# Performance work log

Measured on AMD Instinct MI355X. Metric: run time of the kernel, lower is better.

## Reference

```python
import jax, jax.numpy as jnp
import numpy as np

B = 10      # number of interacting objects
NDIM = 2    # self.n: position/velocity dimensionality

# Edge list equivalent to rel_rec/rel_send one-hot matrices (edges grouped by receiver)
_rec_idx, _send_idx = np.where(~np.eye(B, dtype=bool))


def _mlp(x, W0, b0, W1, b1, W2, b2):
    # MLP with 2 hidden softplus layers, linear output
    h = jax.nn.softplus(x @ W0 + b0)
    h = jax.nn.softplus(h @ W1 + b1)
    return h @ W2 + b2


def setup_inputs() -> dict:
    key = jax.random.key(0)
    ks = jax.random.split(key, 7)
    N = 8192            # trajectories per batch
    H = 128             # hidden width of self-dynamics MLP
    Hi = 128            # hidden width of interaction MLP
    nin = 2 * NDIM      # self MLP input dim (pos+vel)
    nout = 2 * NDIM     # n_f_out for order=1
    nin_i = 3 * NDIM    # interaction MLP input dim (p1-p2, v1, v2)
    w = lambda k, shp: jax.random.normal(k, shp, jnp.float32) / np.float32(np.sqrt(shp[0]))
    return {
        "z": jax.random.normal(ks[0], (N * B, 2 * NDIM), jnp.float32),
        "fW0": w(ks[1], (nin, H)),   "fb0": jnp.zeros((H,), jnp.float32),
        "fW1": w(ks[2], (H, H)),     "fb1": jnp.zeros((H,), jnp.float32),
        "fW2": w(ks[3], (H, nout)),  "fb2": jnp.zeros((nout,), jnp.float32),
        "iW0": w(ks[4], (nin_i, Hi)),"ib0": jnp.zeros((Hi,), jnp.float32),
        "iW1": w(ks[5], (Hi, Hi)),   "ib1": jnp.zeros((Hi,), jnp.float32),
        "iW2": w(ks[6], (Hi, nout)), "ib2": jnp.zeros((nout,), jnp.float32),
    }


def reference(z, fW0, fb0, fW1, fb1, fW2, fb2, iW0, ib0, iW1, ib1, iW2, ib2):
    # One evaluation of the ODE vector field (order=1, n_aug_dyn=n_aug_st=0).
    n = NDIM
    NB = z.shape[0]
    N = NB // B
    dz_self = _mlp(z, fW0, fb0, fW1, fb1, fW2, fb2)            # [N*B, 2n]
    z3 = z.reshape(N, B, 2 * n)
    recv = z3[:, _rec_idx]                                     # [N, B(B-1), 2n] gather (node2edge)
    send = z3[:, _send_idx]
    # odefint input: (p_recv - p_send, v_recv, v_send)  -> [N, B(B-1), 3n]
    inp = jnp.concatenate([recv[..., :n] - send[..., :n], recv[..., n:], send[..., n:]], -1)
    dz_int = _mlp(inp, iW0, ib0, iW1, ib1, iW2, ib2)           # [N, B(B-1), 2n]
    dz_int = dz_int.reshape(N, B, B - 1, 2 * n).sum(2)         # sum over senders per receiver
    dz = dz_self.reshape(N, B, 2 * n) + dz_int
    return dz.reshape(NB, 2 * n)
```

## Files before the change

kernel.cpp:

```cpp
#include <hip/hip_runtime.h>
#include <hip/hip_bf16.h>

#define NDIM 2
#define BB 10
#define H 128
#define PAIRS 90
#define MROWS 128
#define LDH 136
#define USLD 132
#define LOG2E 1.4426950408889634f
#define LN2   0.6931471805599453f

typedef short short8 __attribute__((ext_vector_type(8)));
typedef float floatx2 __attribute__((ext_vector_type(2)));
typedef float floatx4 __attribute__((ext_vector_type(4)));
typedef float floatx16 __attribute__((ext_vector_type(16)));

__device__ inline short f2bf(float x) {
    unsigned u = __float_as_uint(x);
    return (short)((u + 0x7fffu + ((u >> 16) & 1u)) >> 16);
}

#if __has_builtin(__builtin_amdgcn_cvt_pk_bf16_f32)
typedef __bf16 bf16x2_t __attribute__((ext_vector_type(2)));
__device__ inline unsigned pk2(float a, float b) {
    bf16x2_t v = __builtin_amdgcn_cvt_pk_bf16_f32(a, b);
    return __builtin_bit_cast(unsigned, v);
}
#else
__device__ inline unsigned pk2(float a, float b) {
    unsigned ua = __float_as_uint(a), ub = __float_as_uint(b);
    ua = (ua + 0x7fffu + ((ua >> 16) & 1u)) >> 16;
    ub = (ub + 0x7fffu + ((ub >> 16) & 1u)) & 0xffff0000u;
    return ua | ub;
}
#endif

__device__ inline float ex2(float x) {
#if __has_builtin(__builtin_amdgcn_exp2f)
    return __builtin_amdgcn_exp2f(x);
#else
    return exp2f(x);
#endif
}

__device__ inline floatx4 sp4(floatx4 xs) {
    floatx4 m, t;
    m[0] = fmaxf(xs[0], 0.f); m[1] = fmaxf(xs[1], 0.f);
    m[2] = fmaxf(xs[2], 0.f); m[3] = fmaxf(xs[3], 0.f);
    t[0] = ex2(fminf(xs[0], -xs[0])); t[1] = ex2(fminf(xs[1], -xs[1]));
    t[2] = ex2(fminf(xs[2], -xs[2])); t[3] = ex2(fminf(xs[3], -xs[3]));
    floatx4 q = t * (t * 0.2057f - 0.6484f) + 1.4426950f;
    return t * q + m;
}

__global__ void prep_weights(const float* __restrict__ iW1, const float* __restrict__ fW1,
                             const float* __restrict__ iW2, const float* __restrict__ fW2,
                             const float* __restrict__ ib1, const float* __restrict__ fb1,
                             const float* __restrict__ iW0, const float* __restrict__ ib0,
                             const float* __restrict__ fW0, const float* __restrict__ fb0,
                             short* __restrict__ W1Fi, short* __restrict__ W1Ff,
                             short* __restrict__ W2Fi, short* __restrict__ W2Ff,
                             float* __restrict__ scal) {
    int t = blockIdx.x * blockDim.x + threadIdx.x;
    int stride = gridDim.x * blockDim.x;
    for (int fidx = t; fidx < 16384; fidx += stride) {
        int j = fidx & 7, lane = (fidx >> 3) & 63, nt = (fidx >> 9) & 3, ks = fidx >> 11;
        int k = 16 * ks + ((lane >> 5) << 3) + j;
        int n = 32 * nt + (lane & 31);
        W1Fi[fidx] = f2bf(iW1[k * H + n]);
        W1Ff[fidx] = f2bf(fW1[k * H + n]);
    }
    for (int fidx = t; fidx < 2048; fidx += stride) {
        int j = fidx & 7, lane = (fidx >> 3) & 63, ks = fidx >> 9;
        int k = 32 * ks + ((lane >> 4) << 3) + j;
        int n = lane & 15;
        W2Fi[fidx] = (n < 4) ? f2bf(iW2[k * 4 + n] * LN2) : (short)0;
        W2Ff[fidx] = (n < 4) ? f2bf(fW2[k * 4 + n] * LN2) : (short)0;
    }
    if (t < 128) {
        scal[t] = ib1[t] * LOG2E;
        scal[128 + t] = fb1[t] * LOG2E;
        scal[1024 + t] = ib0[t] * LOG2E;
        scal[1664 + t] = fb0[t] * LOG2E;
    }
    if (t < 768) scal[256 + t] = iW0[t] * LOG2E;
    if (t < 512) scal[1152 + t] = fW0[t] * LOG2E;
}

__global__ __launch_bounds__(512, 6) void fused_kernel(
    const float* __restrict__ z,
    const float* __restrict__ ib2, const float* __restrict__ fb2,
    const short* __restrict__ W1Fi, const short* __restrict__ W2Fi,
    const short* __restrict__ W1Ff, const short* __restrict__ W2Ff,
    const float* __restrict__ scal, float* __restrict__ out) {
    __shared__ __align__(16) short h0s[MROWS * LDH];
    __shared__ __align__(16) float uws[2 * BB * USLD];
    __shared__ __align__(16) float4 zs4[BB];
    float* us   = uws;
    float* wss  = uws + BB * USLD;
    float* outs = uws;

    int n = blockIdx.x;
    int tid = threadIdx.x, lane = tid & 63, wave = tid >> 6;
    int c31 = lane & 31, halfk = lane >> 5;
    int ntw = wave & 3, mhalf = wave >> 2;

    short8 af[8];
#pragma unroll
    for (int ks = 0; ks < 8; ++ks)
        af[ks] = *(const short8*)(W1Fi + ((ks * 4 + ntw) * 64 + lane) * 8);

    if (tid < BB) zs4[tid] = ((const float4*)z)[n * BB + tid];
    __syncthreads();

    {
        const float* iW0s = scal + 256;
        for (int u = tid; u < 640; u += 512) {
            int b = u >> 6, c2 = (u & 63) * 2;
            float4 zb = zs4[b];
            floatx2 p0 = *(const floatx2*)(iW0s + c2);
            floatx2 p1 = *(const floatx2*)(iW0s + 128 + c2);
            floatx2 p2 = *(const floatx2*)(iW0s + 256 + c2);
            floatx2 p3 = *(const floatx2*)(iW0s + 384 + c2);
            floatx2 p4 = *(const floatx2*)(iW0s + 512 + c2);
            floatx2 p5 = *(const floatx2*)(iW0s + 640 + c2);
            floatx2 pb = *(const floatx2*)(scal + 1024 + c2);
            floatx2 s = p0 * zb.x + p1 * zb.y;
            floatx2 uv = pb + s + p2 * zb.z + p3 * zb.w;
            floatx2 wv = p4 * zb.z + p5 * zb.w - s;
            *(floatx2*)(us + b * USLD + c2) = uv;
            *(floatx2*)(wss + b * USLD + c2) = wv;
        }
    }
    if (tid < 320) {
        int b = tid >> 5, c4 = (tid & 31) * 4;
        const float* fW0s = scal + 1152;
        float4 zb = zs4[b];
        floatx4 q0 = *(const floatx4*)(fW0s + c4);
        floatx4 q1 = *(const floatx4*)(fW0s + 128 + c4);
        floatx4 q2 = *(const floatx4*)(fW0s + 256 + c4);
        floatx4 q3 = *(const floatx4*)(fW0s + 384 + c4);
        floatx4 qb = *(const floatx4*)(scal + 1664 + c4);
        floatx4 a = qb + q0 * zb.x + q1 * zb.y + q2 * zb.z + q3 * zb.w;
        floatx4 g = sp4(a);
        uint2 pk;
        pk.x = pk2(g[0], g[1]);
        pk.y = pk2(g[2], g[3]);
        *(uint2*)(h0s + (96 + b) * LDH + c4) = pk;
    }
    if (tid < 352) {
        int r = 106 + (tid >> 4), c8 = (tid & 15) * 8;
        *(uint4*)(h0s + r * LDH + c8) = uint4{0u, 0u, 0u, 0u};
    }
    __syncthreads();

    {
        int m0 = tid >> 4, c8 = (tid & 15) * 8;
#pragma unroll
        for (int t = 0; t < 3; ++t) {
            int m = m0 + 32 * t;
            uint4 o = {0u, 0u, 0u, 0u};
            if (m < PAIRS) {
                int i = (m * 57) >> 9;
                int s = m - 9 * i;
                int j = s + (s >= i);
                floatx4 ua = *(const floatx4*)(us + i * USLD + c8);
                floatx4 ub = *(const floatx4*)(us + i * USLD + c8 + 4);
                floatx4 wa = *(const floatx4*)(wss + j * USLD + c8);
                floatx4 wb = *(const floatx4*)(wss + j * USLD + c8 + 4);
                floatx4 ga = sp4(ua + wa);
                floatx4 gb = sp4(ub + wb);
                o.x = pk2(ga[0], ga[1]);
                o.y = pk2(ga[2], ga[3]);
                o.z = pk2(gb[0], gb[1]);
                o.w = pk2(gb[2], gb[3]);
            }
            *(uint4*)(h0s + m * LDH + c8) = o;
        }
    }
    __syncthreads();

    int hb = 32 * ntw + 4 * halfk;
    floatx16 acc0, acc1;
    {
        const float* blo_ = scal;
        const float* bhi_ = mhalf ? (scal + 128) : scal;
#pragma unroll
        for (int g = 0; g < 4; ++g) {
            float4 v0 = *(const float4*)(blo_ + hb + 8 * g);
            float4 v1 = *(const float4*)(bhi_ + hb + 8 * g);
            acc0[4 * g + 0] = v0.x; acc0[4 * g + 1] = v0.y;
            acc0[4 * g + 2] = v0.z; acc0[4 * g + 3] = v0.w;
            acc1[4 * g + 0] = v1.x; acc1[4 * g + 1] = v1.y;
            acc1[4 * g + 2] = v1.z; acc1[4 * g + 3] = v1.w;
        }
    }
    int rowA = 64 * mhalf + c31;
    int rowB = rowA + 32;
#pragma unroll
    for (int ks = 0; ks < 8; ++ks) {
        short8 bf = *(const short8*)(h0s + rowA * LDH + 16 * ks + 8 * halfk);
        acc0 = __builtin_amdgcn_mfma_f32_32x32x16_bf16(af[ks], bf, acc0, 0, 0, 0);
    }
    if (mhalf) {
#pragma unroll
        for (int ks = 0; ks < 8; ++ks)
            af[ks] = *(const short8*)(W1Ff + ((ks * 4 + ntw) * 64 + lane) * 8);
    }
#pragma unroll
    for (int ks = 0; ks < 8; ++ks) {
        short8 bf = *(const short8*)(h0s + rowB * LDH + 16 * ks + 8 * halfk);
        acc1 = __builtin_amdgcn_mfma_f32_32x32x16_bf16(af[ks], bf, acc1, 0, 0, 0);
    }
    __syncthreads();

#pragma unroll
    for (int g = 0; g < 4; ++g) {
        floatx4 v0 = {acc0[4 * g], acc0[4 * g + 1], acc0[4 * g + 2], acc0[4 * g + 3]};
        floatx4 v1 = {acc1[4 * g], acc1[4 * g + 1], acc1[4 * g + 2], acc1[4 * g + 3]};
        floatx4 r0 = sp4(v0);
        floatx4 r1 = sp4(v1);
        uint2 pa, pb;
        pa.x = pk2(r0[0], r0[1]); pa.y = pk2(r0[2], r0[3]);
        pb.x = pk2(r1[0], r1[1]); pb.y = pk2(r1[2], r1[3]);
        *(uint2*)(h0s + rowA * LDH + 32 * ntw + 8 * g + 4 * halfk) = pa;
        *(uint2*)(h0s + rowB * LDH + 32 * ntw + 8 * g + 4 * halfk) = pb;
    }
    __syncthreads();

    {
        int rit = lane & 15, quad = lane >> 4;
        if (wave < 7) {
            const short* W2 = (wave == 6) ? W2Ff : W2Fi;
            const float* b2 = (wave == 6) ? fb2 : ib2;
            floatx4 a = {0.f, 0.f, 0.f, 0.f};
            if (quad == 0) {
                float4 bbv = *(const float4*)b2;
                a = floatx4{bbv.x, bbv.y, bbv.z, bbv.w};
            }
#pragma unroll
            for (int ks = 0; ks < 4; ++ks) {
                short8 w2v = *(const short8*)(W2 + (ks * 64 + lane) * 8);
                short8 bf = *(const short8*)(h0s + (16 * wave + rit) * LDH + 32 * ks + quad * 8);
                a = __builtin_amdgcn_mfma_f32_16x16x32_bf16(w2v, bf, a, 0, 0, 0);
            }
            if (quad == 0) {
                float4 o = {a[0], a[1], a[2], a[3]};
                *(float4*)(outs + (16 * wave + rit) * 4) = o;
            }
        }
    }
    __syncthreads();

    if (tid < BB * 4) {
        int i = tid >> 2, c = tid & 3;
        float s = outs[(96 + i) * 4 + c];
#pragma unroll
        for (int p = 0; p < 9; ++p) s += outs[(9 * i + p) * 4 + c];
        out[(n * BB + i) * 4 + c] = s;
    }
}

extern "C" void kernel_launch(void* const* d_in, const int* in_sizes, int n_in,
                              void* d_out, int out_size, void* d_ws, size_t ws_size,
                              hipStream_t stream) {
    const float* z   = (const float*)d_in[0];
    const float* fW0 = (const float*)d_in[1];
    const float* fb0 = (const float*)d_in[2];
    const float* fW1 = (const float*)d_in[3];
    const float* fb1 = (const float*)d_in[4];
    const float* fW2 = (const float*)d_in[5];
    const float* fb2 = (const float*)d_in[6];
    const float* iW0 = (const float*)d_in[7];
    const float* ib0 = (const float*)d_in[8];
    const float* iW1 = (const float*)d_in[9];
    const float* ib1 = (const float*)d_in[10];
    const float* iW2 = (const float*)d_in[11];
    const float* ib2 = (const float*)d_in[12];
    float* out = (float*)d_out;

    short* wsS = (short*)d_ws;
    short* W1Fi = wsS;
    short* W1Ff = wsS + 16384;
    short* W2Fi = wsS + 32768;
    short* W2Ff = wsS + 34816;
    float* scal = (float*)(wsS + 36864);

    int NB = in_sizes[0] / (2 * NDIM);
    int Nsys = NB / BB;

    hipLaunchKernelGGL(prep_weights, dim3(128), dim3(256), 0, stream,
                       iW1, fW1, iW2, fW2, ib1, fb1, iW0, ib0, fW0, fb0,
                       W1Fi, W1Ff, W2Fi, W2Ff, scal);
    hipLaunchKernelGGL(fused_kernel, dim3(Nsys), dim3(512), 0, stream,
                       z, ib2, fb2, W1Fi, W2Fi, W1Ff, W2Ff, scal, out);
}
```

Baseline: 181.0 us.

## Cheapen softplus, drop staging sync and padding writes, coalesce weight prep

```diff
diff --git a/kernel.cpp b/kernel.cpp
--- a/kernel.cpp
+++ b/kernel.cpp
@@ -44,13 +44,22 @@
 #endif
 }
 
+#define SP_C0 1.4038f
+#define SP_C1 (-0.4167f)
+
+__device__ inline float sp1(float xs) {
+    float m = fmaxf(xs, 0.f);
+    float t = ex2(fminf(xs, -xs));
+    return fmaf(t, fmaf(t, SP_C1, SP_C0), m);
+}
+
 __device__ inline floatx4 sp4(floatx4 xs) {
     floatx4 m, t;
     m[0] = fmaxf(xs[0], 0.f); m[1] = fmaxf(xs[1], 0.f);
     m[2] = fmaxf(xs[2], 0.f); m[3] = fmaxf(xs[3], 0.f);
     t[0] = ex2(fminf(xs[0], -xs[0])); t[1] = ex2(fminf(xs[1], -xs[1]));
     t[2] = ex2(fminf(xs[2], -xs[2])); t[3] = ex2(fminf(xs[3], -xs[3]));
-    floatx4 q = t * (t * 0.2057f - 0.6484f) + 1.4426950f;
+    floatx4 q = t * SP_C1 + SP_C0;
     return t * q + m;
 }
 
@@ -64,12 +73,13 @@
                              float* __restrict__ scal) {
     int t = blockIdx.x * blockDim.x + threadIdx.x;
     int stride = gridDim.x * blockDim.x;
-    for (int fidx = t; fidx < 16384; fidx += stride) {
-        int j = fidx & 7, lane = (fidx >> 3) & 63, nt = (fidx >> 9) & 3, ks = fidx >> 11;
-        int k = 16 * ks + ((lane >> 5) << 3) + j;
-        int n = 32 * nt + (lane & 31);
-        W1Fi[fidx] = f2bf(iW1[k * H + n]);
-        W1Ff[fidx] = f2bf(fW1[k * H + n]);
+    for (int idx = t; idx < 16384; idx += stride) {
+        int k = idx >> 7, n = idx & 127;
+        int nt = n >> 5, c31 = n & 31;
+        int ks = k >> 4, halfk = (k >> 3) & 1, j = k & 7;
+        int fidx = ((((ks * 4 + nt) * 2 + halfk) * 32 + c31) << 3) + j;
+        W1Fi[fidx] = f2bf(iW1[idx]);
+        W1Ff[fidx] = f2bf(fW1[idx]);
     }
     for (int fidx = t; fidx < 2048; fidx += stride) {
         int j = fidx & 7, lane = (fidx >> 3) & 63, ks = fidx >> 9;
@@ -96,7 +106,6 @@
     const float* __restrict__ scal, float* __restrict__ out) {
     __shared__ __align__(16) short h0s[MROWS * LDH];
     __shared__ __align__(16) float uws[2 * BB * USLD];
-    __shared__ __align__(16) float4 zs4[BB];
     float* us   = uws;
     float* wss  = uws + BB * USLD;
     float* outs = uws;
@@ -105,20 +114,18 @@
     int tid = threadIdx.x, lane = tid & 63, wave = tid >> 6;
     int c31 = lane & 31, halfk = lane >> 5;
     int ntw = wave & 3, mhalf = wave >> 2;
+    const float4* zrow = (const float4*)(z + n * (BB * 4));
 
     short8 af[8];
 #pragma unroll
     for (int ks = 0; ks < 8; ++ks)
         af[ks] = *(const short8*)(W1Fi + ((ks * 4 + ntw) * 64 + lane) * 8);
-
-    if (tid < BB) zs4[tid] = ((const float4*)z)[n * BB + tid];
-    __syncthreads();
 
     {
         const float* iW0s = scal + 256;
         for (int u = tid; u < 640; u += 512) {
             int b = u >> 6, c2 = (u & 63) * 2;
-            float4 zb = zs4[b];
+            float4 zb = zrow[b];
             floatx2 p0 = *(const floatx2*)(iW0s + c2);
             floatx2 p1 = *(const floatx2*)(iW0s + 128 + c2);
             floatx2 p2 = *(const floatx2*)(iW0s + 256 + c2);
@@ -133,25 +140,19 @@
             *(floatx2*)(wss + b * USLD + c2) = wv;
         }
     }
-    if (tid < 320) {
-        int b = tid >> 5, c4 = (tid & 31) * 4;
+    {
         const float* fW0s = scal + 1152;
-        float4 zb = zs4[b];
-        floatx4 q0 = *(const floatx4*)(fW0s + c4);
-        floatx4 q1 = *(const floatx4*)(fW0s + 128 + c4);
-        floatx4 q2 = *(const floatx4*)(fW0s + 256 + c4);
-        floatx4 q3 = *(const floatx4*)(fW0s + 384 + c4);
-        floatx4 qb = *(const floatx4*)(scal + 1664 + c4);
-        floatx4 a = qb + q0 * zb.x + q1 * zb.y + q2 * zb.z + q3 * zb.w;
-        floatx4 g = sp4(a);
-        uint2 pk;
-        pk.x = pk2(g[0], g[1]);
-        pk.y = pk2(g[2], g[3]);
-        *(uint2*)(h0s + (96 + b) * LDH + c4) = pk;
-    }
-    if (tid < 352) {
-        int r = 106 + (tid >> 4), c8 = (tid & 15) * 8;
-        *(uint4*)(h0s + r * LDH + c8) = uint4{0u, 0u, 0u, 0u};
+        for (int u = tid; u < 640; u += 512) {
+            int b = u >> 6, c2 = (u & 63) * 2;
+            float4 zb = zrow[b];
+            floatx2 q0 = *(const floatx2*)(fW0s + c2);
+            floatx2 q1 = *(const floatx2*)(fW0s + 128 + c2);
+            floatx2 q2 = *(const floatx2*)(fW0s + 256 + c2);
+            floatx2 q3 = *(const floatx2*)(fW0s + 384 + c2);
+            floatx2 qb = *(const floatx2*)(scal + 1664 + c2);
+            floatx2 a = qb + q0 * zb.x + q1 * zb.y + q2 * zb.z + q3 * zb.w;
+            *(unsigned*)(h0s + (96 + b) * LDH + c2) = pk2(sp1(a[0]), sp1(a[1]));
+        }
     }
     __syncthreads();
 
@@ -160,22 +161,21 @@
 #pragma unroll
         for (int t = 0; t < 3; ++t) {
             int m = m0 + 32 * t;
-            uint4 o = {0u, 0u, 0u, 0u};
-            if (m < PAIRS) {
-                int i = (m * 57) >> 9;
-                int s = m - 9 * i;
-                int j = s + (s >= i);
-                floatx4 ua = *(const floatx4*)(us + i * USLD + c8);
-                floatx4 ub = *(const floatx4*)(us + i * USLD + c8 + 4);
-                floatx4 wa = *(const floatx4*)(wss + j * USLD + c8);
-                floatx4 wb = *(const floatx4*)(wss + j * USLD + c8 + 4);
-                floatx4 ga = sp4(ua + wa);
-                floatx4 gb = sp4(ub + wb);
-                o.x = pk2(ga[0], ga[1]);
-                o.y = pk2(ga[2], ga[3]);
-                o.z = pk2(gb[0], gb[1]);
-                o.w = pk2(gb[2], gb[3]);
-            }
+            if (t == 2 && m0 >= 26) break;
+            int i = (m * 57) >> 9;
+            int s = m - 9 * i;
+            int j = s + (s >= i);
+            floatx4 ua = *(const floatx4*)(us + i * USLD + c8);
+            floatx4 ub = *(const floatx4*)(us + i * USLD + c8 + 4);
+            floatx4 wa = *(const floatx4*)(wss + j * USLD + c8);
+            floatx4 wb = *(const floatx4*)(wss + j * USLD + c8 + 4);
+            floatx4 ga = sp4(ua + wa);
+            floatx4 gb = sp4(ub + wb);
+            uint4 o;
+            o.x = pk2(ga[0], ga[1]);
+            o.y = pk2(ga[2], ga[3]);
+            o.z = pk2(gb[0], gb[1]);
+            o.w = pk2(gb[2], gb[3]);
             *(uint4*)(h0s + m * LDH + c8) = o;
         }
     }
```

New measurement: 190.3 us. 5.2% more time.
